# Performance work log

Measured on AMD Instinct MI355X. Metric: run time of the kernel, lower is better.

Reference implementation:

```python
import jax, jax.numpy as jnp
import numpy as np

B, T, D = 8, 2048, 256  # batch, time segments, feature dim (a_dim=v_dim=hidden=out=256)
EPS = 1e-8


def _layer_norm(x, g, b, eps=1e-6):
    m = jnp.mean(x, axis=-1, keepdims=True)
    v = jnp.var(x, axis=-1, keepdims=True)
    return (x - m) * jax.lax.rsqrt(v + eps) * g + b


def setup_inputs() -> dict:
    key = jax.random.key(0)
    ks = jax.random.split(key, 9)
    xav = lambda k: jax.random.uniform(k, (D, D), jnp.float32, -1.0, 1.0) * np.sqrt(6.0 / (D + D))
    return {
        "a_fea": jax.random.normal(ks[0], (B, T, D), jnp.float32),
        "v_fea": jax.random.normal(ks[1], (B, T, D), jnp.float32),
        "thr_val": jnp.float32(0.099),
        "Wv1": xav(ks[2]), "Wv2": xav(ks[3]), "Wvfc": xav(ks[4]),
        "Wa1": xav(ks[5]), "Wa2": xav(ks[6]), "Wafc": xav(ks[7]),
        "ln_g": jnp.ones((D,), jnp.float32),
        "ln_b": jnp.zeros((D,), jnp.float32),
    }


def reference(a_fea, v_fea, thr_val, Wv1, Wv2, Wvfc, Wa1, Wa2, Wafc, ln_g, ln_b):
    relu = jax.nn.relu
    # branch projections (dropout is identity at eval); torch Linear: x @ W.T
    v1 = relu(jnp.einsum('btd,hd->bth', v_fea, Wv1))
    v2 = relu(jnp.einsum('btd,hd->bth', v_fea, Wv2))
    a1 = relu(jnp.einsum('btd,hd->bth', a_fea, Wa1))
    a2 = relu(jnp.einsum('btd,hd->bth', a_fea, Wa2))

    d = v2.shape[-1]
    # scaled cross-modal scores, ReLU'd  [B, Tv, Ta]
    beta_va = relu(jnp.einsum('btd,bsd->bts', v2, a1) / jnp.sqrt(jnp.float32(d)))
    # a->v scores taken BEFORE row-normalization of beta_va (as in torch code)
    beta_av = jnp.transpose(beta_va, (0, 2, 1))

    time = beta_va.shape[-1]
    thr = thr_val * 10.0 / time

    # normalize -> threshold sparsify -> renormalize (v attends to a)
    bn_va = beta_va / (jnp.sum(beta_va, axis=-1, keepdims=True) + EPS)
    g_va = jnp.where(bn_va > thr, bn_va, 0.0)
    g_va = g_va / (jnp.sum(g_va, axis=-1, keepdims=True) + EPS)

    # same for a attends to v
    bn_av = beta_av / (jnp.sum(beta_av, axis=-1, keepdims=True) + EPS)
    g_av = jnp.where(bn_av > thr, bn_av, 0.0)
    g_av = g_av / (jnp.sum(g_av, axis=-1, keepdims=True) + EPS)

    # vectorized form of the diagonal selection double-loop (batch element 0)
    pred = (jnp.diagonal(g_av[0]) > 0).astype(jnp.float32)  # [T]

    a_pos = jnp.einsum('bts,bsd->btd', g_va, a2)
    v_psp = v_fea + a_pos
    v_pos = jnp.einsum('bts,bsd->btd', g_av, v1)
    a_psp = a_fea + v_pos

    v_psp = _layer_norm(relu(jnp.einsum('btd,od->bto', v_psp, Wvfc)), ln_g, ln_b)
    a_psp = _layer_norm(relu(jnp.einsum('btd,od->bto', a_psp, Wafc)), ln_g, ln_b)
    a_v_fuse = 0.5 * (v_psp + a_psp)
    return a_v_fuse, v_psp, a_psp, pred
```

## Files before the change

### kernel.cpp

```cpp
#include <hip/hip_runtime.h>
#include <math.h>

#define TT 2048
#define DD 256
#define NBATCH 8
#define EPSF 1e-8f

typedef unsigned short u16;
typedef __attribute__((ext_vector_type(8))) short short8;
typedef __attribute__((ext_vector_type(4))) float f32x4;

__device__ __forceinline__ u16 f2bf(float x) {
    unsigned int u = __builtin_bit_cast(unsigned int, x);
    u += 0x7fffu + ((u >> 16) & 1u);
    return (u16)(u >> 16);
}
__device__ __forceinline__ float bf2f(u16 h) {
    return __builtin_bit_cast(float, (unsigned int)h << 16);
}

__device__ __forceinline__ int frag_dst(int row, int k) {
    return (((row >> 4) * 4 + (k >> 3)) * 16 + (row & 15)) * 8 + (k & 7);
}

__device__ __forceinline__ int swz(int i) { return i ^ ((i >> 2) & 32); }

template<int BR>
__device__ __forceinline__ void stage_tile(const u16* __restrict__ g, u16* s,
                                           int row0, int k0, int ldk, int tid)
{
    #pragma unroll
    for (int i = 0; i < BR / 64; ++i) {
        const int c = tid + 256 * i;
        const int row = c >> 2, q = c & 3;
        *(int4*)(s + swz(frag_dst(row, q * 8))) =
            *(const int4*)(g + (long)(row0 + row) * ldk + k0 + q * 8);
    }
}

__global__ __launch_bounds__(256)
void proj_kernel(const u16* __restrict__ vfh, const u16* __restrict__ vfl,
                 const u16* __restrict__ afh, const u16* __restrict__ afl,
                 const u16* __restrict__ Wsp,
                 u16* __restrict__ v2h, u16* __restrict__ v2l,
                 u16* __restrict__ a1h, u16* __restrict__ a1l,
                 u16* __restrict__ v1T, u16* __restrict__ a2T)
{
    const int zz = blockIdx.z;
    const u16* Ah = (zz == 1 || zz == 3) ? afh : vfh;
    const u16* Al = (zz == 1 || zz == 3) ? afl : vfl;
    const int widx = (zz == 0) ? 2 : (zz == 1) ? 4 : (zz == 2) ? 0 : 6;
    const u16* Bh = Wsp + widx * DD * DD;
    const u16* Bl = Bh + DD * DD;
    const bool split = zz < 2;
    u16* Oh = (zz == 0) ? v2h : a1h;
    u16* Ol = (zz == 0) ? v2l : a1l;
    u16* OT = (zz == 2) ? v1T : a2T;

    __shared__ __align__(16) u16 Ah_s[64 * 32], Al_s[64 * 32];
    __shared__ __align__(16) u16 Bh_s[64 * 32], Bl_s[64 * 32];
    const int m0 = blockIdx.y * 64, n0 = blockIdx.x * 64;
    const int tid = threadIdx.x, lane = tid & 63, w = tid >> 6;
    const int wy = w >> 1, wx = w & 1;
    f32x4 acc[2][2] = {};

    for (int k0 = 0; k0 < DD; k0 += 32) {
        stage_tile<64>(Ah, Ah_s, m0, k0, DD, tid);
        stage_tile<64>(Al, Al_s, m0, k0, DD, tid);
        stage_tile<64>(Bh, Bh_s, n0, k0, DD, tid);
        stage_tile<64>(Bl, Bl_s, n0, k0, DD, tid);
        __syncthreads();
        short8 ah[2], al[2], bh[2], bl[2];
        #pragma unroll
        for (int i = 0; i < 2; ++i) {
            ah[i] = *(const short8*)(Ah_s + swz(((wy * 2 + i) * 64 + lane) * 8));
            al[i] = *(const short8*)(Al_s + swz(((wy * 2 + i) * 64 + lane) * 8));
        }
        #pragma unroll
        for (int j = 0; j < 2; ++j) {
            bh[j] = *(const short8*)(Bh_s + swz(((wx * 2 + j) * 64 + lane) * 8));
            bl[j] = *(const short8*)(Bl_s + swz(((wx * 2 + j) * 64 + lane) * 8));
        }
        #pragma unroll
        for (int i = 0; i < 2; ++i)
            #pragma unroll
            for (int j = 0; j < 2; ++j) {
                acc[i][j] = __builtin_amdgcn_mfma_f32_16x16x32_bf16(ah[i], bl[j], acc[i][j], 0, 0, 0);
                acc[i][j] = __builtin_amdgcn_mfma_f32_16x16x32_bf16(al[i], bh[j], acc[i][j], 0, 0, 0);
                acc[i][j] = __builtin_amdgcn_mfma_f32_16x16x32_bf16(ah[i], bh[j], acc[i][j], 0, 0, 0);
            }
        __syncthreads();
    }
    const int quad = lane >> 4, col = lane & 15;
    #pragma unroll
    for (int i = 0; i < 2; ++i)
        #pragma unroll
        for (int j = 0; j < 2; ++j) {
            const int c = n0 + (wx * 2 + j) * 16 + col;
            const int rbase = m0 + (wy * 2 + i) * 16 + quad * 4;
            if (split) {
                #pragma unroll
                for (int r = 0; r < 4; ++r) {
                    const float v = fmaxf(acc[i][j][r], 0.f);
                    const u16 h = f2bf(v);
                    Oh[(long)(rbase + r) * DD + c] = h;
                    Ol[(long)(rbase + r) * DD + c] = f2bf(v - bf2f(h));
                }
            } else {
                short4 pk;
                pk.x = (short)f2bf(fmaxf(acc[i][j][0], 0.f));
                pk.y = (short)f2bf(fmaxf(acc[i][j][1], 0.f));
                pk.z = (short)f2bf(fmaxf(acc[i][j][2], 0.f));
                pk.w = (short)f2bf(fmaxf(acc[i][j][3], 0.f));
                const int b = rbase >> 11, t = rbase & (TT - 1);
                *(short4*)(OT + ((long)b * DD + c) * TT + t) = pk;
            }
        }
}

__global__ __launch_bounds__(512)
void score_kernel(const u16* __restrict__ v2h, const u16* __restrict__ v2l,
                  const u16* __restrict__ a1h, const u16* __restrict__ a1l,
                  u16* __restrict__ beta, u16* __restrict__ betaT,
                  float* __restrict__ rs, float* __restrict__ cs)
{
    __shared__ __align__(16) u16 S[128 * 136];
    u16* Ah_s = S;
    u16* Al_s = S + 4096;
    u16* Bh_s = S + 8192;
    u16* Bl_s = S + 12288;
    const int z = blockIdx.z;
    const int m0 = blockIdx.y * 128, n0 = blockIdx.x * 128;
    const int tid = threadIdx.x, lane = tid & 63, w = tid >> 6;
    const int wy = w >> 2, wx = w & 3;
    const long zoff = (long)z * TT * DD;
    f32x4 acc[4][2] = {};

    const int prow = tid >> 2, pq = tid & 3;
    const int d0 = swz(frag_dst(prow, pq * 8));
    const u16* gAh = v2h + zoff + (long)(m0 + prow) * DD + pq * 8;
    const u16* gAl = v2l + zoff + (long)(m0 + prow) * DD + pq * 8;
    const u16* gBh = a1h + zoff + (long)(n0 + prow) * DD + pq * 8;
    const u16* gBl = a1l + zoff + (long)(n0 + prow) * DD + pq * 8;

    int4 rAh = *(const int4*)(gAh);
    int4 rAl = *(const int4*)(gAl);
    int4 rBh = *(const int4*)(gBh);
    int4 rBl = *(const int4*)(gBl);

    for (int k0 = 0; k0 < DD; k0 += 32) {
        *(int4*)(Ah_s + d0) = rAh;
        *(int4*)(Al_s + d0) = rAl;
        *(int4*)(Bh_s + d0) = rBh;
        *(int4*)(Bl_s + d0) = rBl;
        __syncthreads();
        const int kn = (k0 + 32 < DD) ? k0 + 32 : 0;
        rAh = *(const int4*)(gAh + kn);
        rAl = *(const int4*)(gAl + kn);
        rBh = *(const int4*)(gBh + kn);
        rBl = *(const int4*)(gBl + kn);
        short8 ah[4], al[4], bh[2], bl[2];
        #pragma unroll
        for (int i = 0; i < 4; ++i) {
            ah[i] = *(const short8*)(Ah_s + swz(((wy * 4 + i) * 64 + lane) * 8));
            al[i] = *(const short8*)(Al_s + swz(((wy * 4 + i) * 64 + lane) * 8));
        }
        #pragma unroll
        for (int j = 0; j < 2; ++j) {
            bh[j] = *(const short8*)(Bh_s + swz(((wx * 2 + j) * 64 + lane) * 8));
            bl[j] = *(const short8*)(Bl_s + swz(((wx * 2 + j) * 64 + lane) * 8));
        }
        #pragma unroll
        for (int i = 0; i < 4; ++i)
            #pragma unroll
            for (int j = 0; j < 2; ++j) {
                acc[i][j] = __builtin_amdgcn_mfma_f32_16x16x32_bf16(ah[i], bl[j], acc[i][j], 0, 0, 0);
                acc[i][j] = __builtin_amdgcn_mfma_f32_16x16x32_bf16(al[i], bh[j], acc[i][j], 0, 0, 0);
                acc[i][j] = __builtin_amdgcn_mfma_f32_16x16x32_bf16(ah[i], bh[j], acc[i][j], 0, 0, 0);
            }
        __syncthreads();
    }

    const int quad = lane >> 4, col = lane & 15;
    const float scale = 1.f / 16.f;
    #pragma unroll
    for (int i = 0; i < 4; ++i)
        #pragma unroll
        for (int j = 0; j < 2; ++j)
            #pragma unroll
            for (int r = 0; r < 4; ++r)
                acc[i][j][r] = fmaxf(acc[i][j][r] * scale, 0.f);

    #pragma unroll
    for (int i = 0; i < 4; ++i) {
        const int rl = (wy * 4 + i) * 16 + quad * 4;
        #pragma unroll
        for (int j = 0; j < 2; ++j) {
            const int cl = (wx * 2 + j) * 16 + col;
            #pragma unroll
            for (int r = 0; r < 4; ++r)
                S[(rl + r) * 136 + cl] = f2bf(acc[i][j][r]);
        }
    }
    __syncthreads();
    #pragma unroll
    for (int it = 0; it < 4; ++it) {
        const int idx = tid + 512 * it;
        const int rl = idx >> 4, cq = idx & 15;
        const int4 v = *(const int4*)(S + rl * 136 + cq * 8);
        *(int4*)(beta + ((long)z * TT + m0 + rl) * TT + n0 + cq * 8) = v;
    }
    #pragma unroll
    for (int i = 0; i < 4; ++i)
        #pragma unroll
        for (int r = 0; r < 4; ++r) {
            float rp = acc[i][0][r] + acc[i][1][r];
            rp += __shfl_xor(rp, 1); rp += __shfl_xor(rp, 2);
            rp += __shfl_xor(rp, 4); rp += __shfl_xor(rp, 8);
            if (col == 0) {
                const int row = m0 + (wy * 4 + i) * 16 + quad * 4 + r;
                atomicAdd(&rs[(long)z * TT + row], rp);
            }
        }
    #pragma unroll
    for (int j = 0; j < 2; ++j) {
        float cp = 0.f;
        #pragma unroll
        for (int i = 0; i < 4; ++i)
            #pragma unroll
            for (int r = 0; r < 4; ++r) cp += acc[i][j][r];
        cp += __shfl_xor(cp, 16); cp += __shfl_xor(cp, 32);
        if (lane < 16) {
            const int c = n0 + (wx * 2 + j) * 16 + col;
            atomicAdd(&cs[(long)z * TT + c], cp);
        }
    }
    __syncthreads();
    #pragma unroll
    for (int i = 0; i < 4; ++i)
        #pragma unroll
        for (int j = 0; j < 2; ++j) {
            const int cl = (wx * 2 + j) * 16 + col;
            const int rl = (wy * 4 + i) * 16 + quad * 4;
            short4 pk;
            pk.x = (short)f2bf(acc[i][j][0]);
            pk.y = (short)f2bf(acc[i][j][1]);
            pk.z = (short)f2bf(acc[i][j][2]);
            pk.w = (short)f2bf(acc[i][j][3]);
            *(short4*)(S + cl * 136 + rl) = pk;
        }
    __syncthreads();
    #pragma unroll
    for (int it = 0; it < 4; ++it) {
        const int idx = tid + 512 * it;
        const int cl = idx >> 4, tq = idx & 15;
        const int4 v = *(const int4*)(S + cl * 136 + tq * 8);
        *(int4*)(betaT + ((long)z * TT + n0 + cl) * TT + m0 + tq * 8) = v;
    }
}

__global__ __launch_bounds__(512)
void pv_kernel(const u16* __restrict__ beta, const u16* __restrict__ betaT,
               const u16* __restrict__ a2T, const u16* __restrict__ v1T,
               const float* __restrict__ rs, const float* __restrict__ cs,
               const float* __restrict__ thrp,
               const float* __restrict__ v_fea, const float* __restrict__ a_fea,
               u16* __restrict__ yvin, u16* __restrict__ yain)
{
    __shared__ __align__(16) u16 A_s[128 * 32], B_s[256 * 32];
    __shared__ float sthr[128], sA[128], ssum[128];
    const int zz = blockIdx.x;
    const int m0 = blockIdx.y * 128;
    const int z = zz & 7;
    const bool av = zz >= 8;
    const u16* P      = av ? betaT : beta;
    const u16* VT     = av ? v1T : a2T;
    const float* sums = av ? cs : rs;
    const float* resid = av ? a_fea : v_fea;
    u16* outb         = av ? yain : yvin;

    const int tid = threadIdx.x, lane = tid & 63, w = tid >> 6;
    const int wy = w >> 2, wx = w & 3;
    const float thr = thrp[0] * 10.0f / (float)TT;
    if (tid < 128) {
        const float s = sums[(long)z * TT + m0 + tid];
        sA[tid] = s; sthr[tid] = thr * (s + EPSF); ssum[tid] = 0.f;
    }
    __syncthreads();
    f32x4 acc[4][4] = {};
    float rpart = 0.f;
    const int arow = tid >> 2, aq = tid & 3;
    const u16* Pp = P + ((long)z * TT + m0 + arow) * TT + aq * 8;
    const u16* V0 = VT + (long)z * DD * TT + (long)arow * TT + aq * 8;
    const u16* V1 = V0 + (long)128 * TT;
    const int da  = swz(frag_dst(arow, aq * 8));
    const int db1 = swz(frag_dst(arow + 128, aq * 8));

    int4 Ar  = *(const int4*)(Pp);
    int4 Br0 = *(const int4*)(V0);
    int4 Br1 = *(const int4*)(V1);

    for (int k0 = 0; k0 < TT; k0 += 32) {
        union { int4 v; u16 us[8]; } U;
        U.v = Ar;
        const float ct = sthr[arow];
        float ss = 0.f;
        #pragma unroll
        for (int t = 0; t < 8; ++t) {
            const float v = bf2f(U.us[t]);
            if (v > ct) ss += v; else U.us[t] = 0;
        }
        rpart += ss;
        *(int4*)(A_s + da) = U.v;
        *(int4*)(B_s + da) = Br0;
        *(int4*)(B_s + db1) = Br1;
        __syncthreads();
        const int kn = (k0 + 32 < TT) ? (k0 + 32) : k0;
        Ar  = *(const int4*)(Pp + kn);
        Br0 = *(const int4*)(V0 + kn);
        Br1 = *(const int4*)(V1 + kn);
        short8 a[4], b[4];
        #pragma unroll
        for (int i = 0; i < 4; ++i)
            a[i] = *(const short8*)(A_s + swz(((wy * 4 + i) * 64 + lane) * 8));
        #pragma unroll
        for (int j = 0; j < 4; ++j)
            b[j] = *(const short8*)(B_s + swz(((wx * 4 + j) * 64 + lane) * 8));
        #pragma unroll
        for (int i = 0; i < 4; ++i)
            #pragma unroll
            for (int j = 0; j < 4; ++j)
                acc[i][j] = __builtin_amdgcn_mfma_f32_16x16x32_bf16(a[i], b[j], acc[i][j], 0, 0, 0);
        __syncthreads();
    }
    atomicAdd(&ssum[arow], rpart);
    __syncthreads();

    const int quad = lane >> 4, col = lane & 15;
    #pragma unroll
    for (int i = 0; i < 4; ++i)
        #pragma unroll
        for (int j = 0; j < 4; ++j) {
            const int c = (wx * 4 + j) * 16 + col;
            #pragma unroll
            for (int r = 0; r < 4; ++r) {
                const int lrow = (wy * 4 + i) * 16 + quad * 4 + r;
                const int row = m0 + lrow;
                const float inv = 1.0f / (ssum[lrow] + EPSF * (sA[lrow] + EPSF));
                const float v = acc[i][j][r] * inv + resid[((long)z * TT + row) * DD + c];
                outb[((long)z * TT + row) * DD + c] = f2bf(v);
            }
        }
}

__global__ __launch_bounds__(256)
void fc_kernel(const u16* __restrict__ Ain, const u16* __restrict__ Wb,
               u16* __restrict__ Cb)
{
    const int z = blockIdx.z;
    const u16* A = Ain + (size_t)z * (size_t)NBATCH * TT * DD;
    const u16* B = Wb + (size_t)z * DD * DD;
    u16* C = Cb + (size_t)z * (size_t)NBATCH * TT * DD;
    __shared__ __align__(16) u16 A_s[128 * 32], B_s[64 * 32];
    const int m0 = blockIdx.y * 128, n0 = blockIdx.x * 64;
    const int tid = threadIdx.x, lane = tid & 63, w = tid >> 6;
    const int wy = w >> 1, wx = w & 1;
    f32x4 acc[4][2] = {};
    for (int k0 = 0; k0 < DD; k0 += 32) {
        stage_tile<128>(A, A_s, m0, k0, DD, tid);
        stage_tile<64>(B, B_s, n0, k0, DD, tid);
        __syncthreads();
        short8 a[4], b[2];
        #pragma unroll
        for (int i = 0; i < 4; ++i)
            a[i] = *(const short8*)(A_s + swz(((wy * 4 + i) * 64 + lane) * 8));
        #pragma unroll
        for (int j = 0; j < 2; ++j)
            b[j] = *(const short8*)(B_s + swz(((wx * 2 + j) * 64 + lane) * 8));
        #pragma unroll
        for (int i = 0; i < 4; ++i)
            #pragma unroll
            for (int j = 0; j < 2; ++j)
                acc[i][j] = __builtin_amdgcn_mfma_f32_16x16x32_bf16(a[i], b[j], acc[i][j], 0, 0, 0);
        __syncthreads();
    }
    const int quad = lane >> 4, col = lane & 15;
    #pragma unroll
    for (int i = 0; i < 4; ++i)
        #pragma unroll
        for (int j = 0; j < 2; ++j) {
            const int c = n0 + (wx * 2 + j) * 16 + col;
            #pragma unroll
            for (int r = 0; r < 4; ++r) {
                const int row = m0 + (wy * 4 + i) * 16 + quad * 4 + r;
                C[(long)row * DD + c] = f2bf(fmaxf(acc[i][j][r], 0.f));
            }
        }
}

__global__ __launch_bounds__(256)
void pred_exact(const float* __restrict__ vf, const float* __restrict__ af,
                const float* __restrict__ Wv2, const float* __restrict__ Wa1,
                const float* __restrict__ cs, const float* __restrict__ thrp,
                float* __restrict__ pred)
{
    __shared__ float vs[8][260];
    __shared__ float as_[8][260];
    __shared__ float red[4][8];
    const int t0 = blockIdx.x * 8;
    const int tid = threadIdx.x;
    {
        const int i = tid >> 5, c = (tid & 31) * 8;
        *(float4*)&vs[i][c] = *(const float4*)(vf + (long)(t0 + i) * DD + c);
        *(float4*)&vs[i][c + 4] = *(const float4*)(vf + (long)(t0 + i) * DD + c + 4);
        *(float4*)&as_[i][c] = *(const float4*)(af + (long)(t0 + i) * DD + c);
        *(float4*)&as_[i][c + 4] = *(const float4*)(af + (long)(t0 + i) * DD + c + 4);
    }
    __syncthreads();
    const int j = tid;
    float av[8] = {0.f}, aa[8] = {0.f};
    for (int k = 0; k < DD; k += 4) {
        const float4 wv = *(const float4*)(Wv2 + (long)j * DD + k);
        const float4 wa = *(const float4*)(Wa1 + (long)j * DD + k);
        #pragma unroll
        for (int i = 0; i < 8; ++i) {
            const float4 x = *(const float4*)&vs[i][k];
            av[i] += wv.x * x.x + wv.y * x.y + wv.z * x.z + wv.w * x.w;
            const float4 y = *(const float4*)&as_[i][k];
            aa[i] += wa.x * y.x + wa.y * y.y + wa.z * y.z + wa.w * y.w;
        }
    }
    float p[8];
    #pragma unroll
    for (int i = 0; i < 8; ++i)
        p[i] = fmaxf(av[i], 0.f) * fmaxf(aa[i], 0.f);
    #pragma unroll
    for (int off = 32; off > 0; off >>= 1)
        #pragma unroll
        for (int i = 0; i < 8; ++i) p[i] += __shfl_xor(p[i], off);
    const int lane = tid & 63, wv_ = tid >> 6;
    if (lane == 0)
        #pragma unroll
        for (int i = 0; i < 8; ++i) red[wv_][i] = p[i];
    __syncthreads();
    if (tid < 8) {
        float d = red[0][tid] + red[1][tid] + red[2][tid] + red[3][tid];
        d = fmaxf(d * (1.f / 16.f), 0.f);
        const float thr = thrp[0] * 10.0f / (float)TT;
        pred[t0 + tid] = (d > thr * (cs[t0 + tid] + EPSF)) ? 1.0f : 0.0f;
    }
}

__global__ __launch_bounds__(256)
void split_feat(const float* __restrict__ vf, const float* __restrict__ af,
                u16* __restrict__ vfh, u16* __restrict__ vfl,
                u16* __restrict__ afh, u16* __restrict__ afl)
{
    const long i4 = ((long)blockIdx.x * 256 + threadIdx.x) * 4;
    const float* src = blockIdx.y ? af : vf;
    u16* dh = blockIdx.y ? afh : vfh;
    u16* dl = blockIdx.y ? afl : vfl;
    float4 a = *(const float4*)(src + i4);
    ushort4 h4, l4; u16 h;
    h = f2bf(a.x); h4.x = h; l4.x = f2bf(a.x - bf2f(h));
    h = f2bf(a.y); h4.y = h; l4.y = f2bf(a.y - bf2f(h));
    h = f2bf(a.z); h4.z = h; l4.z = f2bf(a.z - bf2f(h));
    h = f2bf(a.w); h4.w = h; l4.w = f2bf(a.w - bf2f(h));
    *(ushort4*)(dh + i4) = h4;
    *(ushort4*)(dl + i4) = l4;
}

__global__ __launch_bounds__(256)
void split_w(const float* __restrict__ w0, const float* __restrict__ w1,
             const float* __restrict__ w2, const float* __restrict__ w3,
             const float* __restrict__ w4, const float* __restrict__ w5,
             u16* __restrict__ out)
{
    const int t = blockIdx.y;
    const float* w = (t == 0) ? w0 : (t == 1) ? w1 : (t == 2) ? w2
                   : (t == 3) ? w3 : (t == 4) ? w4 : w5;
    const int i4 = (blockIdx.x * 256 + threadIdx.x) * 4;
    float4 a = *(const float4*)(w + i4);
    if (t < 4) {
        u16* oh = out + (size_t)t * 2 * DD * DD;
        u16* ol = oh + DD * DD;
        ushort4 h4, l4; u16 h;
        h = f2bf(a.x); h4.x = h; l4.x = f2bf(a.x - bf2f(h));
        h = f2bf(a.y); h4.y = h; l4.y = f2bf(a.y - bf2f(h));
        h = f2bf(a.z); h4.z = h; l4.z = f2bf(a.z - bf2f(h));
        h = f2bf(a.w); h4.w = h; l4.w = f2bf(a.w - bf2f(h));
        *(ushort4*)(oh + i4) = h4;
        *(ushort4*)(ol + i4) = l4;
    } else {
        u16* ob = out + (size_t)8 * DD * DD + (size_t)(t - 4) * DD * DD;
        ushort4 o;
        o.x = f2bf(a.x); o.y = f2bf(a.y); o.z = f2bf(a.z); o.w = f2bf(a.w);
        *(ushort4*)(ob + i4) = o;
    }
}

__global__ __launch_bounds__(256)
void ln_fuse_kernel(const u16* __restrict__ yv, const u16* __restrict__ ya,
                    const float* __restrict__ g, const float* __restrict__ b,
                    float* __restrict__ fuse, float* __restrict__ vpsp,
                    float* __restrict__ apsp)
{
    const long row = (long)blockIdx.x * 4 + (threadIdx.x >> 6);
    const int lane = threadIdx.x & 63;
    const ushort4 hv = *(const ushort4*)(yv + row * DD + lane * 4);
    const ushort4 ha = *(const ushort4*)(ya + row * DD + lane * 4);
    const float xv0 = bf2f(hv.x), xv1 = bf2f(hv.y), xv2 = bf2f(hv.z), xv3 = bf2f(hv.w);
    const float xa0 = bf2f(ha.x), xa1 = bf2f(ha.y), xa2 = bf2f(ha.z), xa3 = bf2f(ha.w);
    float sv = xv0 + xv1 + xv2 + xv3;
    float sa = xa0 + xa1 + xa2 + xa3;
    #pragma unroll
    for (int off = 32; off > 0; off >>= 1) {
        sv += __shfl_xor(sv, off);
        sa += __shfl_xor(sa, off);
    }
    const float mv = sv * (1.f / 256.f);
    const float ma = sa * (1.f / 256.f);
    const float dv0 = xv0 - mv, dv1 = xv1 - mv, dv2 = xv2 - mv, dv3 = xv3 - mv;
    const float da0 = xa0 - ma, da1 = xa1 - ma, da2 = xa2 - ma, da3 = xa3 - ma;
    float qv = dv0 * dv0 + dv1 * dv1 + dv2 * dv2 + dv3 * dv3;
    float qa = da0 * da0 + da1 * da1 + da2 * da2 + da3 * da3;
    #pragma unroll
    for (int off = 32; off > 0; off >>= 1) {
        qv += __shfl_xor(qv, off);
        qa += __shfl_xor(qa, off);
    }
    const float rv = rsqrtf(qv * (1.f / 256.f) + 1e-6f);
    const float ra = rsqrtf(qa * (1.f / 256.f) + 1e-6f);
    const float4 gg = *(const float4*)(g + lane * 4);
    const float4 bb = *(const float4*)(b + lane * 4);
    float4 ov, oa, of;
    ov.x = dv0 * rv * gg.x + bb.x; ov.y = dv1 * rv * gg.y + bb.y;
    ov.z = dv2 * rv * gg.z + bb.z; ov.w = dv3 * rv * gg.w + bb.w;
    oa.x = da0 * ra * gg.x + bb.x; oa.y = da1 * ra * gg.y + bb.y;
    oa.z = da2 * ra * gg.z + bb.z; oa.w = da3 * ra * gg.w + bb.w;
    of.x = 0.5f * (ov.x + oa.x); of.y = 0.5f * (ov.y + oa.y);
    of.z = 0.5f * (ov.z + oa.z); of.w = 0.5f * (ov.w + oa.w);
    *(float4*)(vpsp + row * DD + lane * 4) = ov;
    *(float4*)(apsp + row * DD + lane * 4) = oa;
    *(float4*)(fuse + row * DD + lane * 4) = of;
}

extern "C" void kernel_launch(void* const* d_in, const int* in_sizes, int n_in,
                              void* d_out, int out_size, void* d_ws, size_t ws_size,
                              hipStream_t stream)
{
    const float* a_fea = (const float*)d_in[0];
    const float* v_fea = (const float*)d_in[1];
    const float* thrp  = (const float*)d_in[2];
    const float* Wv1   = (const float*)d_in[3];
    const float* Wv2   = (const float*)d_in[4];
    const float* Wvfc  = (const float*)d_in[5];
    const float* Wa1   = (const float*)d_in[6];
    const float* Wa2   = (const float*)d_in[7];
    const float* Wafc  = (const float*)d_in[8];
    const float* lng   = (const float*)d_in[9];
    const float* lnb   = (const float*)d_in[10];

    const long MT = (long)NBATCH * TT;
    float* out_fuse = (float*)d_out;
    float* out_vpsp = out_fuse + MT * DD;
    float* out_apsp = out_vpsp + MT * DD;
    float* out_pred = out_apsp + MT * DD;

    char* ws = (char*)d_ws;
    const size_t fb = (size_t)MT * DD * sizeof(u16);
    const size_t sumB = (size_t)MT * sizeof(float);
    u16* v2h  = (u16*)(ws + 0 * fb);
    u16* v2l  = (u16*)(ws + 1 * fb);
    u16* a1h  = (u16*)(ws + 2 * fb);
    u16* a1l  = (u16*)(ws + 3 * fb);
    u16* yvin = (u16*)(ws + 4 * fb);
    u16* yain = (u16*)(ws + 5 * fb);
    u16* v1T  = (u16*)(ws + 6 * fb);
    u16* a2T  = (u16*)(ws + 7 * fb);
    char* p = ws + 8 * fb;
    float* rs = (float*)(p + 0 * sumB);
    float* cs = (float*)(p + 1 * sumB);
    u16* Wsp  = (u16*)(p + 2 * sumB);
    char* q = p + 2 * sumB + 10 * DD * DD * sizeof(u16);
    const size_t betaB = (size_t)NBATCH * TT * TT * sizeof(u16);
    u16* beta  = (u16*)q;
    u16* betaT = (u16*)(q + betaB);
    u16* vfh = (u16*)q;
    u16* vfl = vfh + MT * DD;
    u16* afh = vfl + MT * DD;
    u16* afl = afh + MT * DD;
    u16* yvb = (u16*)(ws + 0 * fb);
    u16* yab = yvb + (size_t)MT * DD;

    hipMemsetAsync(rs, 0, 2 * sumB, stream);

    const dim3 blk(256, 1, 1);

    split_feat<<<dim3((unsigned)(MT * DD / 1024), 2, 1), blk, 0, stream>>>(
        v_fea, a_fea, vfh, vfl, afh, afl);
    split_w<<<dim3(DD * DD / 1024, 6, 1), blk, 0, stream>>>(
        Wv1, Wv2, Wa1, Wa2, Wvfc, Wafc, Wsp);

    proj_kernel<<<dim3(DD / 64, (unsigned)(MT / 64), 4), blk, 0, stream>>>(
        vfh, vfl, afh, afl, Wsp, v2h, v2l, a1h, a1l, v1T, a2T);

    score_kernel<<<dim3(TT / 128, TT / 128, NBATCH), dim3(512, 1, 1), 0, stream>>>(
        v2h, v2l, a1h, a1l, beta, betaT, rs, cs);
    pred_exact<<<dim3(TT / 8, 1, 1), blk, 0, stream>>>(
        v_fea, a_fea, Wv2, Wa1, cs, thrp, out_pred);

    pv_kernel<<<dim3(2 * NBATCH, TT / 128, 1), dim3(512, 1, 1), 0, stream>>>(
        beta, betaT, a2T, v1T, rs, cs, thrp, v_fea, a_fea, yvin, yain);

    fc_kernel<<<dim3(DD / 64, (unsigned)(MT / 128), 2), blk, 0, stream>>>(
        yvin, Wsp + 8 * DD * DD, yvb);
    ln_fuse_kernel<<<dim3((unsigned)(MT / 4), 1, 1), blk, 0, stream>>>(
        yvb, yab, lng, lnb, out_fuse, out_vpsp, out_apsp);
}
```

Measured before the change: 402.4 us.

## Enlarge proj tile with register-prefetched staging and prestage bf16 residuals

The projection kernel now uses 512 threads and 128x64 tiles, one global load per thread per operand. The next k-slice is prefetched into registers while the current slice is computed, which replaces the old synchronous staging. Separately, split_feat writes the bf16 high half of each input feature into the yvin/yain buffers. The PV kernel then adds its result to that stored value instead of reading the fp32 residual, which cuts residual read traffic. The residual is now rounded to bf16 before the add, which adds a small extra rounding error.

```diff
diff --git a/kernel.cpp b/kernel.cpp
--- a/kernel.cpp
+++ b/kernel.cpp
@@ -38,7 +38,7 @@
     }
 }
 
-__global__ __launch_bounds__(256)
+__global__ __launch_bounds__(512)
 void proj_kernel(const u16* __restrict__ vfh, const u16* __restrict__ vfl,
                  const u16* __restrict__ afh, const u16* __restrict__ afl,
                  const u16* __restrict__ Wsp,
@@ -57,65 +57,74 @@
     u16* Ol = (zz == 0) ? v2l : a1l;
     u16* OT = (zz == 2) ? v1T : a2T;
 
-    __shared__ __align__(16) u16 Ah_s[64 * 32], Al_s[64 * 32];
+    __shared__ __align__(16) u16 Ah_s[128 * 32], Al_s[128 * 32];
     __shared__ __align__(16) u16 Bh_s[64 * 32], Bl_s[64 * 32];
-    const int m0 = blockIdx.y * 64, n0 = blockIdx.x * 64;
+    const int m0 = blockIdx.y * 128, n0 = blockIdx.x * 64;
     const int tid = threadIdx.x, lane = tid & 63, w = tid >> 6;
-    const int wy = w >> 1, wx = w & 1;
-    f32x4 acc[2][2] = {};
+    const int wy = w >> 2, wx = w & 3;
+    f32x4 acc[4] = {};
+
+    const int prow = tid >> 2, pq = tid & 3;
+    const int dA = swz(frag_dst(prow, pq * 8));
+    const u16* gAh = Ah + (long)(m0 + prow) * DD + pq * 8;
+    const u16* gAl = Al + (long)(m0 + prow) * DD + pq * 8;
+    const int brow = (tid & 255) >> 2, bq = tid & 3;
+    const int dB = swz(frag_dst(brow, bq * 8));
+    const u16* gB = ((tid < 256) ? Bh : Bl) + (long)(n0 + brow) * DD + bq * 8;
+    u16* sB = (tid < 256) ? Bh_s : Bl_s;
+
+    int4 rAh = *(const int4*)(gAh);
+    int4 rAl = *(const int4*)(gAl);
+    int4 rB  = *(const int4*)(gB);
 
     for (int k0 = 0; k0 < DD; k0 += 32) {
-        stage_tile<64>(Ah, Ah_s, m0, k0, DD, tid);
-        stage_tile<64>(Al, Al_s, m0, k0, DD, tid);
-        stage_tile<64>(Bh, Bh_s, n0, k0, DD, tid);
-        stage_tile<64>(Bl, Bl_s, n0, k0, DD, tid);
-        __syncthreads();
-        short8 ah[2], al[2], bh[2], bl[2];
-        #pragma unroll
-        for (int i = 0; i < 2; ++i) {
-            ah[i] = *(const short8*)(Ah_s + swz(((wy * 2 + i) * 64 + lane) * 8));
-            al[i] = *(const short8*)(Al_s + swz(((wy * 2 + i) * 64 + lane) * 8));
-        }
-        #pragma unroll
-        for (int j = 0; j < 2; ++j) {
-            bh[j] = *(const short8*)(Bh_s + swz(((wx * 2 + j) * 64 + lane) * 8));
-            bl[j] = *(const short8*)(Bl_s + swz(((wx * 2 + j) * 64 + lane) * 8));
-        }
-        #pragma unroll
-        for (int i = 0; i < 2; ++i)
-            #pragma unroll
-            for (int j = 0; j < 2; ++j) {
-                acc[i][j] = __builtin_amdgcn_mfma_f32_16x16x32_bf16(ah[i], bl[j], acc[i][j], 0, 0, 0);
-                acc[i][j] = __builtin_amdgcn_mfma_f32_16x16x32_bf16(al[i], bh[j], acc[i][j], 0, 0, 0);
-                acc[i][j] = __builtin_amdgcn_mfma_f32_16x16x32_bf16(ah[i], bh[j], acc[i][j], 0, 0, 0);
+        *(int4*)(Ah_s + dA) = rAh;
+        *(int4*)(Al_s + dA) = rAl;
+        *(int4*)(sB + dB)   = rB;
+        __syncthreads();
+        const int kn = (k0 + 32 < DD) ? k0 + 32 : 0;
+        rAh = *(const int4*)(gAh + kn);
+        rAl = *(const int4*)(gAl + kn);
+        rB  = *(const int4*)(gB + kn);
+        short8 ah[4], al[4], bh, bl;
+        #pragma unroll
+        for (int i = 0; i < 4; ++i) {
+            ah[i] = *(const short8*)(Ah_s + swz(((wy * 4 + i) * 64 + lane) * 8));
+            al[i] = *(const short8*)(Al_s + swz(((wy * 4 + i) * 64 + lane) * 8));
+        }
+        bh = *(const short8*)(Bh_s + swz((wx * 64 + lane) * 8));
+        bl = *(const short8*)(Bl_s + swz((wx * 64 + lane) * 8));
+        #pragma unroll
+        for (int i = 0; i < 4; ++i) {
+            acc[i] = __builtin_amdgcn_mfma_f32_16x16x32_bf16(ah[i], bl, acc[i], 0, 0, 0);
+            acc[i] = __builtin_amdgcn_mfma_f32_16x16x32_bf16(al[i], bh, acc[i], 0, 0, 0);
+            acc[i] = __builtin_amdgcn_mfma_f32_16x16x32_bf16(ah[i], bh, acc[i], 0, 0, 0);
+        }
+        __syncthreads();
+    }
+    const int quad = lane >> 4, col = lane & 15;
+    const int c = n0 + wx * 16 + col;
+    #pragma unroll
+    for (int i = 0; i < 4; ++i) {
+        const int rbase = m0 + wy * 64 + i * 16 + quad * 4;
+        if (split) {
+            #pragma unroll
+            for (int r = 0; r < 4; ++r) {
+                const float v = fmaxf(acc[i][r], 0.f);
+                const u16 h = f2bf(v);
+                Oh[(long)(rbase + r) * DD + c] = h;
+                Ol[(long)(rbase + r) * DD + c] = f2bf(v - bf2f(h));
             }
-        __syncthreads();
-    }
-    const int quad = lane >> 4, col = lane & 15;
-    #pragma unroll
-    for (int i = 0; i < 2; ++i)
-        #pragma unroll
-        for (int j = 0; j < 2; ++j) {
-            const int c = n0 + (wx * 2 + j) * 16 + col;
-            const int rbase = m0 + (wy * 2 + i) * 16 + quad * 4;
-            if (split) {
-                #pragma unroll
-                for (int r = 0; r < 4; ++r) {
-                    const float v = fmaxf(acc[i][j][r], 0.f);
-                    const u16 h = f2bf(v);
-                    Oh[(long)(rbase + r) * DD + c] = h;
-                    Ol[(long)(rbase + r) * DD + c] = f2bf(v - bf2f(h));
-                }
-            } else {
-                short4 pk;
-                pk.x = (short)f2bf(fmaxf(acc[i][j][0], 0.f));
-                pk.y = (short)f2bf(fmaxf(acc[i][j][1], 0.f));
-                pk.z = (short)f2bf(fmaxf(acc[i][j][2], 0.f));
-                pk.w = (short)f2bf(fmaxf(acc[i][j][3], 0.f));
-                const int b = rbase >> 11, t = rbase & (TT - 1);
-                *(short4*)(OT + ((long)b * DD + c) * TT + t) = pk;
-            }
-        }
+        } else {
+            short4 pk;
+            pk.x = (short)f2bf(fmaxf(acc[i][0], 0.f));
+            pk.y = (short)f2bf(fmaxf(acc[i][1], 0.f));
+            pk.z = (short)f2bf(fmaxf(acc[i][2], 0.f));
+            pk.w = (short)f2bf(fmaxf(acc[i][3], 0.f));
+            const int b = rbase >> 11, t = rbase & (TT - 1);
+            *(short4*)(OT + ((long)b * DD + c) * TT + t) = pk;
+        }
+    }
 }
 
 __global__ __launch_bounds__(512)
@@ -264,7 +273,6 @@
                const u16* __restrict__ a2T, const u16* __restrict__ v1T,
                const float* __restrict__ rs, const float* __restrict__ cs,
                const float* __restrict__ thrp,
-               const float* __restrict__ v_fea, const float* __restrict__ a_fea,
                u16* __restrict__ yvin, u16* __restrict__ yain)
 {
     __shared__ __align__(16) u16 A_s[128 * 32], B_s[256 * 32];
@@ -276,7 +284,6 @@
     const u16* P      = av ? betaT : beta;
     const u16* VT     = av ? v1T : a2T;
     const float* sums = av ? cs : rs;
-    const float* resid = av ? a_fea : v_fea;
     u16* outb         = av ? yain : yvin;
 
     const int tid = threadIdx.x, lane = tid & 63, w = tid >> 6;
@@ -347,8 +354,9 @@
                 const int lrow = (wy * 4 + i) * 16 + quad * 4 + r;
                 const int row = m0 + lrow;
                 const float inv = 1.0f / (ssum[lrow] + EPSF * (sA[lrow] + EPSF));
-                const float v = acc[i][j][r] * inv + resid[((long)z * TT + row) * DD + c];
-                outb[((long)z * TT + row) * DD + c] = f2bf(v);
+                const long oidx = ((long)z * TT + row) * DD + c;
+                const float v = acc[i][j][r] * inv + bf2f(outb[oidx]);
+                outb[oidx] = f2bf(v);
             }
         }
 }
@@ -454,12 +462,14 @@
 __global__ __launch_bounds__(256)
 void split_feat(const float* __restrict__ vf, const float* __restrict__ af,
                 u16* __restrict__ vfh, u16* __restrict__ vfl,
-                u16* __restrict__ afh, u16* __restrict__ afl)
+                u16* __restrict__ afh, u16* __restrict__ afl,
+                u16* __restrict__ vcp, u16* __restrict__ acp)
 {
     const long i4 = ((long)blockIdx.x * 256 + threadIdx.x) * 4;
     const float* src = blockIdx.y ? af : vf;
     u16* dh = blockIdx.y ? afh : vfh;
     u16* dl = blockIdx.y ? afl : vfl;
+    u16* dc = blockIdx.y ? acp : vcp;
     float4 a = *(const float4*)(src + i4);
     ushort4 h4, l4; u16 h;
     h = f2bf(a.x); h4.x = h; l4.x = f2bf(a.x - bf2f(h));
@@ -468,6 +478,7 @@
     h = f2bf(a.w); h4.w = h; l4.w = f2bf(a.w - bf2f(h));
     *(ushort4*)(dh + i4) = h4;
     *(ushort4*)(dl + i4) = l4;
+    *(ushort4*)(dc + i4) = h4;
 }
 
 __global__ __launch_bounds__(256)
@@ -598,11 +609,11 @@
     const dim3 blk(256, 1, 1);
 
     split_feat<<<dim3((unsigned)(MT * DD / 1024), 2, 1), blk, 0, stream>>>(
-        v_fea, a_fea, vfh, vfl, afh, afl);
+        v_fea, a_fea, vfh, vfl, afh, afl, yvin, yain);
     split_w<<<dim3(DD * DD / 1024, 6, 1), blk, 0, stream>>>(
         Wv1, Wv2, Wa1, Wa2, Wvfc, Wafc, Wsp);
 
-    proj_kernel<<<dim3(DD / 64, (unsigned)(MT / 64), 4), blk, 0, stream>>>(
+    proj_kernel<<<dim3(DD / 64, (unsigned)(MT / 128), 4), dim3(512, 1, 1), 0, stream>>>(
         vfh, vfl, afh, afl, Wsp, v2h, v2l, a1h, a1l, v1T, a2T);
 
     score_kernel<<<dim3(TT / 128, TT / 128, NBATCH), dim3(512, 1, 1), 0, stream>>>(
@@ -611,7 +622,7 @@
         v_fea, a_fea, Wv2, Wa1, cs, thrp, out_pred);
 
     pv_kernel<<<dim3(2 * NBATCH, TT / 128, 1), dim3(512, 1, 1), 0, stream>>>(
-        beta, betaT, a2T, v1T, rs, cs, thrp, v_fea, a_fea, yvin, yain);
+        beta, betaT, a2T, v1T, rs, cs, thrp, yvin, yain);
 
     fc_kernel<<<dim3(DD / 64, (unsigned)(MT / 128), 2), blk, 0, stream>>>(
         yvin, Wsp + 8 * DD * DD, yvb);
```

Result: no change. 407.2 us (+1.2%).
